# Kernel optimization log

Hardware: AMD Instinct MI355X
Metric: run time of the kernel (lower is better)

Reference implementation:

```python
import jax, jax.numpy as jnp
import numpy as np

N_HEAD = 16
SCALE = True


def setup_inputs() -> dict:
    key = jax.random.key(0)
    k1, k2, k3 = jax.random.split(key, 3)
    B, S, D = 4, 2048, 1024
    x = jax.random.normal(k1, (B, S, D), dtype=jnp.float32)
    w_attn = jax.random.normal(k2, (D, 3 * D), dtype=jnp.float32) * 0.02
    b_attn = jnp.zeros((3 * D,), dtype=jnp.float32)
    w_proj = jax.random.normal(k3, (D, D), dtype=jnp.float32) * 0.02
    b_proj = jnp.zeros((D,), dtype=jnp.float32)
    return {"x": x, "w_attn": w_attn, "b_attn": b_attn, "w_proj": w_proj, "b_proj": b_proj}


def reference(x, w_attn, b_attn, w_proj, b_proj):
    B, S, D = x.shape
    H = N_HEAD
    hd = D // H
    qkv = x @ w_attn + b_attn  # [B,S,3D] (Conv1D)
    q, k, v = jnp.split(qkv, 3, axis=-1)
    # split heads -> [B,H,S,hd]
    q = q.reshape(B, S, H, hd).transpose(0, 2, 1, 3)
    k = k.reshape(B, S, H, hd).transpose(0, 2, 1, 3)
    v = v.reshape(B, S, H, hd).transpose(0, 2, 1, 3)
    w = jnp.einsum('bhqd,bhkd->bhqk', q, k)  # [B,H,S,S]
    if SCALE:
        w = w / jnp.sqrt(jnp.asarray(hd, dtype=w.dtype))
    # causal mask exactly as in source: w*b + -10000*(1-b)
    bmask = jnp.tril(jnp.ones((S, S), dtype=w.dtype))[None, None]
    w = w * bmask + (-10000.0) * (1.0 - bmask)
    w = jax.nn.softmax(w, axis=-1)
    a = jnp.einsum('bhqk,bhkd->bhqd', w, v)  # [B,H,S,hd]
    a = a.transpose(0, 2, 1, 3).reshape(B, S, D)  # merge heads
    out = a @ w_proj + b_proj
    return out
```

## Files before the change

kernel.cpp:

```cpp
#include <hip/hip_runtime.h>

typedef __attribute__((ext_vector_type(8))) _Float16 f16x8;
typedef __attribute__((ext_vector_type(4))) float f32x4;

#define S_LEN 2048
#define DMODEL 1024
#define NHEAD 16
#define HD 64
#define QKV_LD 3072
#define BTOT 4
#define LOG2E 1.4426950408889634f

#define GLL16(g, l)                                              \
  __builtin_amdgcn_global_load_lds(                              \
      (const __attribute__((address_space(1))) void*)(g),        \
      (__attribute__((address_space(3))) void*)(l), 16, 0, 0)

#define MFMA16(a, b, c) __builtin_amdgcn_mfma_f32_16x16x32_f16(a, b, c, 0, 0, 0)

__global__ __launch_bounds__(256) void cvt_f32_f16_k(const float* __restrict__ in,
                                                     _Float16* __restrict__ out, int n) {
  int i = (blockIdx.x * 256 + threadIdx.x) * 4;
  int stride = gridDim.x * 256 * 4;
  for (; i < n; i += stride) {
    float4 v = *(const float4*)(in + i);
    _Float16 h[4];
    h[0] = (_Float16)v.x; h[1] = (_Float16)v.y; h[2] = (_Float16)v.z; h[3] = (_Float16)v.w;
    *(uint2*)(out + i) = *(const uint2*)h;
  }
}

__global__ __launch_bounds__(256) void transpose_cvt_k(const float* __restrict__ W,
                                                       _Float16* __restrict__ Wt,
                                                       int K, int N) {
  __shared__ float t[32][33];
  int n0 = blockIdx.x * 32, k0 = blockIdx.y * 32;
  int tx = threadIdx.x, ty = threadIdx.y;
#pragma unroll
  for (int i = 0; i < 32; i += 8)
    t[ty + i][tx] = W[(size_t)(k0 + ty + i) * N + n0 + tx];
  __syncthreads();
#pragma unroll
  for (int i = 0; i < 32; i += 8)
    Wt[(size_t)(n0 + ty + i) * K + k0 + tx] = (_Float16)t[tx][ty + i];
}

template <int OUT_F32>
__global__ __launch_bounds__(256) void gemm_bt_k(const _Float16* __restrict__ A,
                                                 const _Float16* __restrict__ Bt,
                                                 const float* __restrict__ bias,
                                                 void* __restrict__ C,
                                                 int M, int N, int K) {
  __shared__ _Float16 As[128 * 64];
  __shared__ _Float16 Bs[128 * 64];
  const int tid = threadIdx.x;
  const int wid = tid >> 6, lane = tid & 63;
  const int quad = lane >> 4, l16 = lane & 15;
  const int wr = wid >> 1, wc = wid & 1;

  const int lin = blockIdx.y * gridDim.x + blockIdx.x;
  const int width = 8 * gridDim.x;
  const int group = lin / width;
  const int pm = group * 8 + (lin % width) % 8;
  const int pn = (lin % width) / 8;
  const int tm = pm * 128, tn = pn * 128;

  const int row0 = tid >> 3;
  const int xc = 8 * ((tid & 7) ^ (row0 & 7));
  const _Float16* Ag = A + (size_t)(tm + row0) * K + xc;
  const _Float16* Bg = Bt + (size_t)(tn + row0) * K + xc;
  _Float16* AsW = &As[wid * 512];
  _Float16* BsW = &Bs[wid * 512];

  f32x4 acc[4][4] = {};

  for (int k0 = 0; k0 < K; k0 += 64) {
    __syncthreads();
#pragma unroll
    for (int p = 0; p < 4; p++) {
      GLL16(Ag + k0 + (size_t)(32 * p) * K, AsW + 2048 * p);
      GLL16(Bg + k0 + (size_t)(32 * p) * K, BsW + 2048 * p);
    }
    __syncthreads();

#pragma unroll
    for (int ks = 0; ks < 2; ks++) {
      f16x8 af[4], bf[4];
#pragma unroll
      for (int mt = 0; mt < 4; mt++)
        af[mt] = *(const f16x8*)&As[(wr * 64 + mt * 16 + l16) * 64 +
                                    (((ks * 4 + quad) ^ (l16 & 7)) << 3)];
#pragma unroll
      for (int nt = 0; nt < 4; nt++)
        bf[nt] = *(const f16x8*)&Bs[(wc * 64 + nt * 16 + l16) * 64 +
                                    (((ks * 4 + quad) ^ (l16 & 7)) << 3)];
#pragma unroll
      for (int mt = 0; mt < 4; mt++)
#pragma unroll
        for (int nt = 0; nt < 4; nt++)
          acc[mt][nt] = MFMA16(af[mt], bf[nt], acc[mt][nt]);
    }
  }

#pragma unroll
  for (int nt = 0; nt < 4; nt++) {
    int col = tn + wc * 64 + nt * 16 + l16;
    float bv = bias[col];
#pragma unroll
    for (int mt = 0; mt < 4; mt++) {
      int row = tm + wr * 64 + mt * 16 + quad * 4;
#pragma unroll
      for (int r = 0; r < 4; r++) {
        float v = acc[mt][nt][r] + bv;
        if (OUT_F32)
          ((float*)C)[(size_t)(row + r) * N + col] = v;
        else
          ((_Float16*)C)[(size_t)(row + r) * N + col] = (_Float16)v;
      }
    }
  }
}

__global__ __launch_bounds__(256, 3) void attn_k(const _Float16* __restrict__ qkv,
                                                 _Float16* __restrict__ out) {
  __shared__ _Float16 Ks[2][4096];
  __shared__ _Float16 VTs[2][4096];
  __shared__ _Float16 Ps[4][2304];

  const int tid = threadIdx.x, wid = tid >> 6, lane = tid & 63;
  const int quad = lane >> 4, l16 = lane & 15;
  const int bh = blockIdx.x, b = bh >> 4, h = bh & 15;
  const int p = blockIdx.y;
  const _Float16* base = qkv + (size_t)b * S_LEN * QKV_LD + h * HD;

  const int krow = tid >> 3;
  const _Float16* Kg = base + DMODEL + (size_t)krow * QKV_LD +
                       8 * ((tid & 7) ^ (krow & 7));
  const int kp = tid & 31, dbase = (tid >> 5) * 8;
  const _Float16* Vg = base + 2 * DMODEL + (size_t)(2 * kp) * QKV_LD + dbase;

  auto stage_V = [&](int bufi, uint4 v0, uint4 v1) {
    union { uint4 u; _Float16 h[8]; } a, c;
    a.u = v0; c.u = v1;
    uint* VT32 = (uint*)VTs[bufi];
#pragma unroll
    for (int i = 0; i < 8; i++) {
      int d = dbase + i;
      union { _Float16 h[2]; uint u; } w;
      w.h[0] = a.h[i]; w.h[1] = c.h[i];
      VT32[d * 32 + (((kp >> 2) ^ (d & 7)) << 2) + (kp & 3)] = w.u;
    }
  };

  auto run_pass = [&](int qt) {
    f16x8 bq[2][2];
    {
      const _Float16 qs = (_Float16)(0.125f * LOG2E);
#pragma unroll
      for (int nt = 0; nt < 2; nt++)
#pragma unroll
        for (int ks = 0; ks < 2; ks++) {
          union { uint4 u; f16x8 h; } v;
          v.u = *(const uint4*)(base + (size_t)(qt + wid * 32 + nt * 16 + l16) * QKV_LD +
                                ks * 32 + quad * 8);
          bq[nt][ks] = v.h * qs;
        }
    }

    float m_i[2] = {-1e30f, -1e30f}, l_i[2] = {0.f, 0.f};
    f32x4 o[4][2] = {};

    const int qmin_w = qt + wid * 32;
    const int qmax_w = qmin_w + 31;
    const int nj = qt / 64 + 2;

    GLL16(Kg, &Ks[0][wid * 512]);
    GLL16(Kg + (size_t)32 * QKV_LD, &Ks[0][2048 + wid * 512]);
    stage_V(0, *(const uint4*)(Vg), *(const uint4*)(Vg + QKV_LD));
    __syncthreads();

    for (int j = 0; j < nj; j++) {
      const int cur = j & 1, nxt = cur ^ 1;
      const int k0g = j * 64;
      const bool pf = (j + 1 < nj);
      uint4 pv0, pv1;
      if (pf) {
        const int kn = k0g + 64;
        GLL16(Kg + (size_t)kn * QKV_LD, &Ks[nxt][wid * 512]);
        GLL16(Kg + (size_t)(kn + 32) * QKV_LD, &Ks[nxt][2048 + wid * 512]);
        pv0 = *(const uint4*)(Vg + (size_t)kn * QKV_LD);
        pv1 = *(const uint4*)(Vg + (size_t)(kn + 1) * QKV_LD);
      }

      if (k0g <= qmax_w) {
        f32x4 sc[4][2] = {};
#pragma unroll
        for (int ks = 0; ks < 2; ks++) {
#pragma unroll
          for (int mt = 0; mt < 4; mt++) {
            f16x8 ak = *(const f16x8*)&Ks[cur][(mt * 16 + l16) * 64 +
                                               (((ks * 4 + quad) ^ (l16 & 7)) << 3)];
            sc[mt][0] = MFMA16(ak, bq[0][ks], sc[mt][0]);
            sc[mt][1] = MFMA16(ak, bq[1][ks], sc[mt][1]);
          }
        }

        const bool need_mask = (k0g + 63 > qmin_w);
        float alpha[2];
#pragma unroll
        for (int nt = 0; nt < 2; nt++) {
          const int qg = qmin_w + nt * 16 + l16;
          float s[16];
#pragma unroll
          for (int mt = 0; mt < 4; mt++)
#pragma unroll
            for (int r = 0; r < 4; r++) {
              float v = sc[mt][nt][r];
              if (need_mask) {
                int kg = k0g + mt * 16 + quad * 4 + r;
                v = (kg <= qg) ? v : -3.0e38f;
              }
              s[mt * 4 + r] = v;
            }
          float mx = s[0];
#pragma unroll
          for (int i = 1; i < 16; i++) mx = fmaxf(mx, s[i]);
          mx = fmaxf(mx, __shfl_xor(mx, 16, 64));
          mx = fmaxf(mx, __shfl_xor(mx, 32, 64));
          float mnew = fmaxf(m_i[nt], mx);
          alpha[nt] = __builtin_amdgcn_exp2f(m_i[nt] - mnew);
          m_i[nt] = mnew;
          float rs = 0.f;
          _Float16 ph[16];
#pragma unroll
          for (int i = 0; i < 16; i++) {
            float pv = __builtin_amdgcn_exp2f(s[i] - mnew);
            rs += pv;
            ph[i] = (_Float16)pv;
          }
          rs += __shfl_xor(rs, 16, 64);
          rs += __shfl_xor(rs, 32, 64);
          l_i[nt] = l_i[nt] * alpha[nt] + rs;
#pragma unroll
          for (int mt = 0; mt < 4; mt++)
            *(uint2*)&Ps[wid][(nt * 16 + l16) * 72 + mt * 16 + quad * 4] =
                *(uint2*)&ph[mt * 4];
        }
#pragma unroll
        for (int md = 0; md < 4; md++) {
          o[md][0] *= alpha[0];
          o[md][1] *= alpha[1];
        }
#pragma unroll
        for (int ks = 0; ks < 2; ks++) {
          f16x8 bp0 = *(const f16x8*)&Ps[wid][l16 * 72 + ks * 32 + quad * 8];
          f16x8 bp1 = *(const f16x8*)&Ps[wid][(16 + l16) * 72 + ks * 32 + quad * 8];
#pragma unroll
          for (int md = 0; md < 4; md++) {
            f16x8 av = *(const f16x8*)&VTs[cur][(md * 16 + l16) * 64 +
                                                (((ks * 4 + quad) ^ (l16 & 7)) << 3)];
            o[md][0] = MFMA16(av, bp0, o[md][0]);
            o[md][1] = MFMA16(av, bp1, o[md][1]);
          }
        }
      }

      if (pf) stage_V(nxt, pv0, pv1);
      __syncthreads();
    }

#pragma unroll
    for (int nt = 0; nt < 2; nt++) {
      float inv = 1.0f / l_i[nt];
#pragma unroll
      for (int md = 0; md < 4; md++) {
        _Float16 hh[4];
#pragma unroll
        for (int r = 0; r < 4; r++) hh[r] = (_Float16)(o[md][nt][r] * inv);
        *(uint2*)&Ps[wid][(nt * 16 + l16) * 72 + md * 16 + quad * 4] = *(uint2*)hh;
      }
    }
    {
      int r = lane >> 1, ch = (lane & 1) * 32;
      const int qg = qt + wid * 32 + r;
      _Float16* orow = out + (size_t)(b * S_LEN + qg) * DMODEL + h * HD + ch;
#pragma unroll
      for (int i = 0; i < 4; i++)
        *(uint4*)(orow + i * 8) = *(const uint4*)&Ps[wid][r * 72 + ch + i * 8];
    }
  };

  run_pass(p * 128);
  run_pass((15 - p) * 128);
}

extern "C" void kernel_launch(void* const* d_in, const int* in_sizes, int n_in,
                              void* d_out, int out_size, void* d_ws, size_t ws_size,
                              hipStream_t stream) {
  const float* x = (const float*)d_in[0];
  const float* w_attn = (const float*)d_in[1];
  const float* b_attn = (const float*)d_in[2];
  const float* w_proj = (const float*)d_in[3];
  const float* b_proj = (const float*)d_in[4];
  float* outp = (float*)d_out;

  char* ws = (char*)d_ws;
  _Float16* x16 = (_Float16*)ws;
  _Float16* wTa = (_Float16*)(ws + 16777216);
  _Float16* wTp = (_Float16*)(ws + 16777216 + 6291456);
  _Float16* qkv = (_Float16*)(ws + 25165824);
  _Float16* abuf = (_Float16*)(ws + 75497472);

  const int nx = BTOT * S_LEN * DMODEL;

  cvt_f32_f16_k<<<8192, 256, 0, stream>>>(x, x16, nx);
  transpose_cvt_k<<<dim3(QKV_LD / 32, DMODEL / 32), dim3(32, 8), 0, stream>>>(
      w_attn, wTa, DMODEL, QKV_LD);
  transpose_cvt_k<<<dim3(DMODEL / 32, DMODEL / 32), dim3(32, 8), 0, stream>>>(
      w_proj, wTp, DMODEL, DMODEL);

  gemm_bt_k<0><<<dim3(QKV_LD / 128, BTOT * S_LEN / 128), 256, 0, stream>>>(
      x16, wTa, b_attn, qkv, BTOT * S_LEN, QKV_LD, DMODEL);

  attn_k<<<dim3(BTOT * NHEAD, 8), 256, 0, stream>>>(qkv, abuf);

  gemm_bt_k<1><<<dim3(DMODEL / 128, BTOT * S_LEN / 128), 256, 0, stream>>>(
      abuf, wTp, b_proj, outp, BTOT * S_LEN, DMODEL, DMODEL);
}
```

Before: 282.8 us.

## Split attention across eight waves of 16 queries with lazy softmax rescaling

The attention kernel moves from 4 waves handling 32 query rows each to 8 waves handling 16 rows each, with 512 threads per block. K loading is spread over all waves, and V transposed staging is done by the first half of the threads. Rescaling of the online softmax is skipped unless the running max grows by more than a threshold across the whole wave. Conversions now use packed round-toward-zero f16. This adds parallelism and cuts per-wave registers, at the cost of fewer MFMAs per K/V LDS load and more waves sharing each barrier.

```diff
diff --git a/kernel.cpp b/kernel.cpp
--- a/kernel.cpp
+++ b/kernel.cpp
@@ -1,6 +1,7 @@
 #include <hip/hip_runtime.h>
 
 typedef __attribute__((ext_vector_type(8))) _Float16 f16x8;
+typedef __attribute__((ext_vector_type(2))) __fp16 h16x2;
 typedef __attribute__((ext_vector_type(4))) float f32x4;
 
 #define S_LEN 2048
@@ -121,11 +122,11 @@
   }
 }
 
-__global__ __launch_bounds__(256, 3) void attn_k(const _Float16* __restrict__ qkv,
+__global__ __launch_bounds__(512, 4) void attn_k(const _Float16* __restrict__ qkv,
                                                  _Float16* __restrict__ out) {
   __shared__ _Float16 Ks[2][4096];
   __shared__ _Float16 VTs[2][4096];
-  __shared__ _Float16 Ps[4][2304];
+  __shared__ _Float16 Ps[8][1152];
 
   const int tid = threadIdx.x, wid = tid >> 6, lane = tid & 63;
   const int quad = lane >> 4, l16 = lane & 15;
@@ -136,7 +137,8 @@
   const int krow = tid >> 3;
   const _Float16* Kg = base + DMODEL + (size_t)krow * QKV_LD +
                        8 * ((tid & 7) ^ (krow & 7));
-  const int kp = tid & 31, dbase = (tid >> 5) * 8;
+  const bool vstager = (tid < 256);
+  const int kp = tid & 31, dbase = ((tid >> 5) & 7) * 8;
   const _Float16* Vg = base + 2 * DMODEL + (size_t)(2 * kp) * QKV_LD + dbase;
 
   auto stage_V = [&](int bufi, uint4 v0, uint4 v1) {
@@ -153,30 +155,27 @@
   };
 
   auto run_pass = [&](int qt) {
-    f16x8 bq[2][2];
+    f16x8 bq[2];
     {
       const _Float16 qs = (_Float16)(0.125f * LOG2E);
 #pragma unroll
-      for (int nt = 0; nt < 2; nt++)
-#pragma unroll
-        for (int ks = 0; ks < 2; ks++) {
-          union { uint4 u; f16x8 h; } v;
-          v.u = *(const uint4*)(base + (size_t)(qt + wid * 32 + nt * 16 + l16) * QKV_LD +
-                                ks * 32 + quad * 8);
-          bq[nt][ks] = v.h * qs;
-        }
-    }
-
-    float m_i[2] = {-1e30f, -1e30f}, l_i[2] = {0.f, 0.f};
-    f32x4 o[4][2] = {};
-
-    const int qmin_w = qt + wid * 32;
-    const int qmax_w = qmin_w + 31;
+      for (int ks = 0; ks < 2; ks++) {
+        union { uint4 u; f16x8 h; } v;
+        v.u = *(const uint4*)(base + (size_t)(qt + wid * 16 + l16) * QKV_LD +
+                              ks * 32 + quad * 8);
+        bq[ks] = v.h * qs;
+      }
+    }
+
+    float m_i = -1e30f, l_i = 0.f;
+    f32x4 o[4] = {};
+
+    const int qmin_w = qt + wid * 16;
+    const int qmax_w = qmin_w + 15;
     const int nj = qt / 64 + 2;
 
     GLL16(Kg, &Ks[0][wid * 512]);
-    GLL16(Kg + (size_t)32 * QKV_LD, &Ks[0][2048 + wid * 512]);
-    stage_V(0, *(const uint4*)(Vg), *(const uint4*)(Vg + QKV_LD));
+    if (vstager) stage_V(0, *(const uint4*)(Vg), *(const uint4*)(Vg + QKV_LD));
     __syncthreads();
 
     for (int j = 0; j < nj; j++) {
@@ -187,106 +186,106 @@
       if (pf) {
         const int kn = k0g + 64;
         GLL16(Kg + (size_t)kn * QKV_LD, &Ks[nxt][wid * 512]);
-        GLL16(Kg + (size_t)(kn + 32) * QKV_LD, &Ks[nxt][2048 + wid * 512]);
-        pv0 = *(const uint4*)(Vg + (size_t)kn * QKV_LD);
-        pv1 = *(const uint4*)(Vg + (size_t)(kn + 1) * QKV_LD);
+        if (vstager) {
+          pv0 = *(const uint4*)(Vg + (size_t)kn * QKV_LD);
+          pv1 = *(const uint4*)(Vg + (size_t)(kn + 1) * QKV_LD);
+        }
       }
 
       if (k0g <= qmax_w) {
-        f32x4 sc[4][2] = {};
-#pragma unroll
-        for (int ks = 0; ks < 2; ks++) {
+        f32x4 sc[4] = {};
+#pragma unroll
+        for (int ks = 0; ks < 2; ks++)
 #pragma unroll
           for (int mt = 0; mt < 4; mt++) {
             f16x8 ak = *(const f16x8*)&Ks[cur][(mt * 16 + l16) * 64 +
                                                (((ks * 4 + quad) ^ (l16 & 7)) << 3)];
-            sc[mt][0] = MFMA16(ak, bq[0][ks], sc[mt][0]);
-            sc[mt][1] = MFMA16(ak, bq[1][ks], sc[mt][1]);
+            sc[mt] = MFMA16(ak, bq[ks], sc[mt]);
           }
+
+        const bool need_mask = (k0g + 63 > qmin_w);
+        const int qg = qmin_w + l16;
+        float s[16];
+#pragma unroll
+        for (int mt = 0; mt < 4; mt++)
+#pragma unroll
+          for (int r = 0; r < 4; r++) {
+            float v = sc[mt][r];
+            if (need_mask) {
+              int kg = k0g + mt * 16 + quad * 4 + r;
+              v = (kg <= qg) ? v : -3.0e38f;
+            }
+            s[mt * 4 + r] = v;
+          }
+        float t0 = fmaxf(fmaxf(s[0], s[1]), s[2]);
+        float t1 = fmaxf(fmaxf(s[3], s[4]), s[5]);
+        float t2 = fmaxf(fmaxf(s[6], s[7]), s[8]);
+        float t3 = fmaxf(fmaxf(s[9], s[10]), s[11]);
+        float t4 = fmaxf(fmaxf(s[12], s[13]), s[14]);
+        float mx = fmaxf(fmaxf(t0, t1), t2);
+        float my = fmaxf(fmaxf(t3, t4), s[15]);
+        mx = fmaxf(mx, my);
+        mx = fmaxf(mx, __shfl_xor(mx, 16, 64));
+        mx = fmaxf(mx, __shfl_xor(mx, 32, 64));
+
+        if (!__all(mx <= m_i + 8.0f)) {
+          float mnew = fmaxf(m_i, mx);
+          float alpha = __builtin_amdgcn_exp2f(m_i - mnew);
+          m_i = mnew;
+          l_i *= alpha;
+#pragma unroll
+          for (int md = 0; md < 4; md++) o[md] *= alpha;
         }
 
-        const bool need_mask = (k0g + 63 > qmin_w);
-        float alpha[2];
-#pragma unroll
-        for (int nt = 0; nt < 2; nt++) {
-          const int qg = qmin_w + nt * 16 + l16;
-          float s[16];
-#pragma unroll
-          for (int mt = 0; mt < 4; mt++)
-#pragma unroll
-            for (int r = 0; r < 4; r++) {
-              float v = sc[mt][nt][r];
-              if (need_mask) {
-                int kg = k0g + mt * 16 + quad * 4 + r;
-                v = (kg <= qg) ? v : -3.0e38f;
-              }
-              s[mt * 4 + r] = v;
-            }
-          float mx = s[0];
-#pragma unroll
-          for (int i = 1; i < 16; i++) mx = fmaxf(mx, s[i]);
-          mx = fmaxf(mx, __shfl_xor(mx, 16, 64));
-          mx = fmaxf(mx, __shfl_xor(mx, 32, 64));
-          float mnew = fmaxf(m_i[nt], mx);
-          alpha[nt] = __builtin_amdgcn_exp2f(m_i[nt] - mnew);
-          m_i[nt] = mnew;
-          float rs = 0.f;
-          _Float16 ph[16];
-#pragma unroll
-          for (int i = 0; i < 16; i++) {
-            float pv = __builtin_amdgcn_exp2f(s[i] - mnew);
-            rs += pv;
-            ph[i] = (_Float16)pv;
-          }
-          rs += __shfl_xor(rs, 16, 64);
-          rs += __shfl_xor(rs, 32, 64);
-          l_i[nt] = l_i[nt] * alpha[nt] + rs;
-#pragma unroll
-          for (int mt = 0; mt < 4; mt++)
-            *(uint2*)&Ps[wid][(nt * 16 + l16) * 72 + mt * 16 + quad * 4] =
-                *(uint2*)&ph[mt * 4];
+        float pe[16];
+#pragma unroll
+        for (int i = 0; i < 16; i++) pe[i] = __builtin_amdgcn_exp2f(s[i] - m_i);
+        float rs = ((pe[0] + pe[1]) + (pe[2] + pe[3])) +
+                   ((pe[4] + pe[5]) + (pe[6] + pe[7])) +
+                   (((pe[8] + pe[9]) + (pe[10] + pe[11])) +
+                    ((pe[12] + pe[13]) + (pe[14] + pe[15])));
+        rs += __shfl_xor(rs, 16, 64);
+        rs += __shfl_xor(rs, 32, 64);
+        l_i += rs;
+
+#pragma unroll
+        for (int mt = 0; mt < 4; mt++) {
+          union { h16x2 h[2]; uint2 u; } w;
+          w.h[0] = __builtin_amdgcn_cvt_pkrtz(pe[mt * 4 + 0], pe[mt * 4 + 1]);
+          w.h[1] = __builtin_amdgcn_cvt_pkrtz(pe[mt * 4 + 2], pe[mt * 4 + 3]);
+          *(uint2*)&Ps[wid][l16 * 72 + mt * 16 + quad * 4] = w.u;
         }
 #pragma unroll
-        for (int md = 0; md < 4; md++) {
-          o[md][0] *= alpha[0];
-          o[md][1] *= alpha[1];
-        }
-#pragma unroll
         for (int ks = 0; ks < 2; ks++) {
-          f16x8 bp0 = *(const f16x8*)&Ps[wid][l16 * 72 + ks * 32 + quad * 8];
-          f16x8 bp1 = *(const f16x8*)&Ps[wid][(16 + l16) * 72 + ks * 32 + quad * 8];
+          f16x8 bp = *(const f16x8*)&Ps[wid][l16 * 72 + ks * 32 + quad * 8];
 #pragma unroll
           for (int md = 0; md < 4; md++) {
             f16x8 av = *(const f16x8*)&VTs[cur][(md * 16 + l16) * 64 +
                                                 (((ks * 4 + quad) ^ (l16 & 7)) << 3)];
-            o[md][0] = MFMA16(av, bp0, o[md][0]);
-            o[md][1] = MFMA16(av, bp1, o[md][1]);
+            o[md] = MFMA16(av, bp, o[md]);
           }
         }
       }
 
-      if (pf) stage_V(nxt, pv0, pv1);
+      if (pf && vstager) stage_V(nxt, pv0, pv1);
       __syncthreads();
     }
 
-#pragma unroll
-    for (int nt = 0; nt < 2; nt++) {
-      float inv = 1.0f / l_i[nt];
+    {
+      float inv = 1.0f / l_i;
 #pragma unroll
       for (int md = 0; md < 4; md++) {
-        _Float16 hh[4];
-#pragma unroll
-        for (int r = 0; r < 4; r++) hh[r] = (_Float16)(o[md][nt][r] * inv);
-        *(uint2*)&Ps[wid][(nt * 16 + l16) * 72 + md * 16 + quad * 4] = *(uint2*)hh;
-      }
-    }
-    {
-      int r = lane >> 1, ch = (lane & 1) * 32;
-      const int qg = qt + wid * 32 + r;
-      _Float16* orow = out + (size_t)(b * S_LEN + qg) * DMODEL + h * HD + ch;
-#pragma unroll
-      for (int i = 0; i < 4; i++)
-        *(uint4*)(orow + i * 8) = *(const uint4*)&Ps[wid][r * 72 + ch + i * 8];
+        union { h16x2 h[2]; uint2 u; } w;
+        w.h[0] = __builtin_amdgcn_cvt_pkrtz(o[md][0] * inv, o[md][1] * inv);
+        w.h[1] = __builtin_amdgcn_cvt_pkrtz(o[md][2] * inv, o[md][3] * inv);
+        *(uint2*)&Ps[wid][l16 * 72 + md * 16 + quad * 4] = w.u;
+      }
+      int r = lane >> 2, cc = (lane & 3) * 16;
+      const int qg = qt + wid * 16 + r;
+      _Float16* orow = out + (size_t)(b * S_LEN + qg) * DMODEL + h * HD + cc;
+#pragma unroll
+      for (int i = 0; i < 2; i++)
+        *(uint4*)(orow + i * 8) = *(const uint4*)&Ps[wid][r * 72 + cc + i * 8];
     }
   };
 
@@ -322,7 +321,7 @@
   gemm_bt_k<0><<<dim3(QKV_LD / 128, BTOT * S_LEN / 128), 256, 0, stream>>>(
       x16, wTa, b_attn, qkv, BTOT * S_LEN, QKV_LD, DMODEL);
 
-  attn_k<<<dim3(BTOT * NHEAD, 8), 256, 0, stream>>>(qkv, abuf);
+  attn_k<<<dim3(BTOT * NHEAD, 8), 512, 0, stream>>>(qkv, abuf);
 
   gemm_bt_k<1><<<dim3(DMODEL / 128, BTOT * S_LEN / 128), 256, 0, stream>>>(
       abuf, wTp, b_proj, outp, BTOT * S_LEN, DMODEL, DMODEL);
```

After: 275.1 us. 2.7% less time.

## Split paired attention passes into one tile per block with lazy softmax rescale

Applied to the files above, without the earlier changes.

The attention kernel now launches 16 blocks per head, each handling one 128-row query tile, with the largest tiles scheduled first. Previously each block ran two balanced passes. This gives more blocks to fill the CUs but relies on the scheduler for causal load balance. Softmax rescaling now happens only when a wave's row max grows by more than 8 (in log2 units), skipping exp and multiplies on most iterations at the cost of larger unnormalized fp16 values. It also uses packed round-toward-zero conversions, a tree-shaped max/sum, and precomputed V transpose offsets.

```diff
diff --git a/kernel.cpp b/kernel.cpp
--- a/kernel.cpp
+++ b/kernel.cpp
@@ -1,6 +1,7 @@
 #include <hip/hip_runtime.h>
 
 typedef __attribute__((ext_vector_type(8))) _Float16 f16x8;
+typedef __attribute__((ext_vector_type(2))) __fp16 h16x2;
 typedef __attribute__((ext_vector_type(4))) float f32x4;
 
 #define S_LEN 2048
@@ -130,7 +131,8 @@
   const int tid = threadIdx.x, wid = tid >> 6, lane = tid & 63;
   const int quad = lane >> 4, l16 = lane & 15;
   const int bh = blockIdx.x, b = bh >> 4, h = bh & 15;
-  const int p = blockIdx.y;
+  const int tile = 15 - blockIdx.y;
+  const int qt = tile * 128;
   const _Float16* base = qkv + (size_t)b * S_LEN * QKV_LD + h * HD;
 
   const int krow = tid >> 3;
@@ -139,159 +141,180 @@
   const int kp = tid & 31, dbase = (tid >> 5) * 8;
   const _Float16* Vg = base + 2 * DMODEL + (size_t)(2 * kp) * QKV_LD + dbase;
 
+  int voff[8];
+#pragma unroll
+  for (int i = 0; i < 8; i++) {
+    int d = dbase + i;
+    voff[i] = d * 32 + (((kp >> 2) ^ (d & 7)) << 2) + (kp & 3);
+  }
+
   auto stage_V = [&](int bufi, uint4 v0, uint4 v1) {
     union { uint4 u; _Float16 h[8]; } a, c;
     a.u = v0; c.u = v1;
     uint* VT32 = (uint*)VTs[bufi];
 #pragma unroll
     for (int i = 0; i < 8; i++) {
-      int d = dbase + i;
       union { _Float16 h[2]; uint u; } w;
       w.h[0] = a.h[i]; w.h[1] = c.h[i];
-      VT32[d * 32 + (((kp >> 2) ^ (d & 7)) << 2) + (kp & 3)] = w.u;
+      VT32[voff[i]] = w.u;
     }
   };
 
-  auto run_pass = [&](int qt) {
-    f16x8 bq[2][2];
-    {
-      const _Float16 qs = (_Float16)(0.125f * LOG2E);
-#pragma unroll
-      for (int nt = 0; nt < 2; nt++)
-#pragma unroll
-        for (int ks = 0; ks < 2; ks++) {
-          union { uint4 u; f16x8 h; } v;
-          v.u = *(const uint4*)(base + (size_t)(qt + wid * 32 + nt * 16 + l16) * QKV_LD +
-                                ks * 32 + quad * 8);
-          bq[nt][ks] = v.h * qs;
+  f16x8 bq[2][2];
+  {
+    const _Float16 qs = (_Float16)(0.125f * LOG2E);
+#pragma unroll
+    for (int nt = 0; nt < 2; nt++)
+#pragma unroll
+      for (int ks = 0; ks < 2; ks++) {
+        union { uint4 u; f16x8 h; } v;
+        v.u = *(const uint4*)(base + (size_t)(qt + wid * 32 + nt * 16 + l16) * QKV_LD +
+                              ks * 32 + quad * 8);
+        bq[nt][ks] = v.h * qs;
+      }
+  }
+
+  float m_i[2] = {-1e30f, -1e30f}, l_i[2] = {0.f, 0.f};
+  f32x4 o[4][2] = {};
+
+  const int qmin_w = qt + wid * 32;
+  const int qmax_w = qmin_w + 31;
+  const int nj = qt / 64 + 2;
+
+  GLL16(Kg, &Ks[0][wid * 512]);
+  GLL16(Kg + (size_t)32 * QKV_LD, &Ks[0][2048 + wid * 512]);
+  stage_V(0, *(const uint4*)(Vg), *(const uint4*)(Vg + QKV_LD));
+  __syncthreads();
+
+  for (int j = 0; j < nj; j++) {
+    const int cur = j & 1, nxt = cur ^ 1;
+    const int k0g = j * 64;
+    const bool pf = (j + 1 < nj);
+    uint4 pv0, pv1;
+    if (pf) {
+      const int kn = k0g + 64;
+      GLL16(Kg + (size_t)kn * QKV_LD, &Ks[nxt][wid * 512]);
+      GLL16(Kg + (size_t)(kn + 32) * QKV_LD, &Ks[nxt][2048 + wid * 512]);
+      pv0 = *(const uint4*)(Vg + (size_t)kn * QKV_LD);
+      pv1 = *(const uint4*)(Vg + (size_t)(kn + 1) * QKV_LD);
+    }
+
+    if (k0g <= qmax_w) {
+      f32x4 sc[4][2] = {};
+#pragma unroll
+      for (int ks = 0; ks < 2; ks++) {
+#pragma unroll
+        for (int mt = 0; mt < 4; mt++) {
+          f16x8 ak = *(const f16x8*)&Ks[cur][(mt * 16 + l16) * 64 +
+                                             (((ks * 4 + quad) ^ (l16 & 7)) << 3)];
+          sc[mt][0] = MFMA16(ak, bq[0][ks], sc[mt][0]);
+          sc[mt][1] = MFMA16(ak, bq[1][ks], sc[mt][1]);
         }
-    }
-
-    float m_i[2] = {-1e30f, -1e30f}, l_i[2] = {0.f, 0.f};
-    f32x4 o[4][2] = {};
-
-    const int qmin_w = qt + wid * 32;
-    const int qmax_w = qmin_w + 31;
-    const int nj = qt / 64 + 2;
-
-    GLL16(Kg, &Ks[0][wid * 512]);
-    GLL16(Kg + (size_t)32 * QKV_LD, &Ks[0][2048 + wid * 512]);
-    stage_V(0, *(const uint4*)(Vg), *(const uint4*)(Vg + QKV_LD));
+      }
+
+      const bool need_mask = (k0g + 63 > qmin_w);
+      float s[2][16];
+      float mx[2];
+#pragma unroll
+      for (int nt = 0; nt < 2; nt++) {
+        const int qg = qmin_w + nt * 16 + l16;
+#pragma unroll
+        for (int mt = 0; mt < 4; mt++)
+#pragma unroll
+          for (int r = 0; r < 4; r++) {
+            float v = sc[mt][nt][r];
+            if (need_mask) {
+              int kg = k0g + mt * 16 + quad * 4 + r;
+              v = (kg <= qg) ? v : -3.0e38f;
+            }
+            s[nt][mt * 4 + r] = v;
+          }
+        float t0 = fmaxf(fmaxf(s[nt][0], s[nt][1]), s[nt][2]);
+        float t1 = fmaxf(fmaxf(s[nt][3], s[nt][4]), s[nt][5]);
+        float t2 = fmaxf(fmaxf(s[nt][6], s[nt][7]), s[nt][8]);
+        float t3 = fmaxf(fmaxf(s[nt][9], s[nt][10]), s[nt][11]);
+        float t4 = fmaxf(fmaxf(s[nt][12], s[nt][13]), s[nt][14]);
+        float m0 = fmaxf(fmaxf(t0, t1), t2);
+        float m1 = fmaxf(fmaxf(t3, t4), s[nt][15]);
+        float m = fmaxf(m0, m1);
+        m = fmaxf(m, __shfl_xor(m, 16, 64));
+        m = fmaxf(m, __shfl_xor(m, 32, 64));
+        mx[nt] = m;
+      }
+
+      bool grow = (mx[0] > m_i[0] + 8.0f) || (mx[1] > m_i[1] + 8.0f);
+      if (__any(grow)) {
+#pragma unroll
+        for (int nt = 0; nt < 2; nt++) {
+          float mnew = fmaxf(m_i[nt], mx[nt]);
+          float alpha = __builtin_amdgcn_exp2f(m_i[nt] - mnew);
+          m_i[nt] = mnew;
+          l_i[nt] *= alpha;
+#pragma unroll
+          for (int md = 0; md < 4; md++) o[md][nt] *= alpha;
+        }
+      }
+
+#pragma unroll
+      for (int nt = 0; nt < 2; nt++) {
+        float pe[16];
+#pragma unroll
+        for (int i = 0; i < 16; i++)
+          pe[i] = __builtin_amdgcn_exp2f(s[nt][i] - m_i[nt]);
+        float rs = ((pe[0] + pe[1]) + (pe[2] + pe[3])) +
+                   ((pe[4] + pe[5]) + (pe[6] + pe[7])) +
+                   (((pe[8] + pe[9]) + (pe[10] + pe[11])) +
+                    ((pe[12] + pe[13]) + (pe[14] + pe[15])));
+        rs += __shfl_xor(rs, 16, 64);
+        rs += __shfl_xor(rs, 32, 64);
+        l_i[nt] += rs;
+
+#pragma unroll
+        for (int mt = 0; mt < 4; mt++) {
+          union { h16x2 h[2]; uint2 u; } w;
+          w.h[0] = __builtin_amdgcn_cvt_pkrtz(pe[mt * 4 + 0], pe[mt * 4 + 1]);
+          w.h[1] = __builtin_amdgcn_cvt_pkrtz(pe[mt * 4 + 2], pe[mt * 4 + 3]);
+          *(uint2*)&Ps[wid][(nt * 16 + l16) * 72 + mt * 16 + quad * 4] = w.u;
+        }
+      }
+
+#pragma unroll
+      for (int ks = 0; ks < 2; ks++) {
+        f16x8 bp0 = *(const f16x8*)&Ps[wid][l16 * 72 + ks * 32 + quad * 8];
+        f16x8 bp1 = *(const f16x8*)&Ps[wid][(16 + l16) * 72 + ks * 32 + quad * 8];
+#pragma unroll
+        for (int md = 0; md < 4; md++) {
+          f16x8 av = *(const f16x8*)&VTs[cur][(md * 16 + l16) * 64 +
+                                              (((ks * 4 + quad) ^ (l16 & 7)) << 3)];
+          o[md][0] = MFMA16(av, bp0, o[md][0]);
+          o[md][1] = MFMA16(av, bp1, o[md][1]);
+        }
+      }
+    }
+
+    if (pf) stage_V(nxt, pv0, pv1);
     __syncthreads();
-
-    for (int j = 0; j < nj; j++) {
-      const int cur = j & 1, nxt = cur ^ 1;
-      const int k0g = j * 64;
-      const bool pf = (j + 1 < nj);
-      uint4 pv0, pv1;
-      if (pf) {
-        const int kn = k0g + 64;
-        GLL16(Kg + (size_t)kn * QKV_LD, &Ks[nxt][wid * 512]);
-        GLL16(Kg + (size_t)(kn + 32) * QKV_LD, &Ks[nxt][2048 + wid * 512]);
-        pv0 = *(const uint4*)(Vg + (size_t)kn * QKV_LD);
-        pv1 = *(const uint4*)(Vg + (size_t)(kn + 1) * QKV_LD);
-      }
-
-      if (k0g <= qmax_w) {
-        f32x4 sc[4][2] = {};
-#pragma unroll
-        for (int ks = 0; ks < 2; ks++) {
-#pragma unroll
-          for (int mt = 0; mt < 4; mt++) {
-            f16x8 ak = *(const f16x8*)&Ks[cur][(mt * 16 + l16) * 64 +
-                                               (((ks * 4 + quad) ^ (l16 & 7)) << 3)];
-            sc[mt][0] = MFMA16(ak, bq[0][ks], sc[mt][0]);
-            sc[mt][1] = MFMA16(ak, bq[1][ks], sc[mt][1]);
-          }
-        }
-
-        const bool need_mask = (k0g + 63 > qmin_w);
-        float alpha[2];
-#pragma unroll
-        for (int nt = 0; nt < 2; nt++) {
-          const int qg = qmin_w + nt * 16 + l16;
-          float s[16];
-#pragma unroll
-          for (int mt = 0; mt < 4; mt++)
-#pragma unroll
-            for (int r = 0; r < 4; r++) {
-              float v = sc[mt][nt][r];
-              if (need_mask) {
-                int kg = k0g + mt * 16 + quad * 4 + r;
-                v = (kg <= qg) ? v : -3.0e38f;
-              }
-              s[mt * 4 + r] = v;
-            }
-          float mx = s[0];
-#pragma unroll
-          for (int i = 1; i < 16; i++) mx = fmaxf(mx, s[i]);
-          mx = fmaxf(mx, __shfl_xor(mx, 16, 64));
-          mx = fmaxf(mx, __shfl_xor(mx, 32, 64));
-          float mnew = fmaxf(m_i[nt], mx);
-          alpha[nt] = __builtin_amdgcn_exp2f(m_i[nt] - mnew);
-          m_i[nt] = mnew;
-          float rs = 0.f;
-          _Float16 ph[16];
-#pragma unroll
-          for (int i = 0; i < 16; i++) {
-            float pv = __builtin_amdgcn_exp2f(s[i] - mnew);
-            rs += pv;
-            ph[i] = (_Float16)pv;
-          }
-          rs += __shfl_xor(rs, 16, 64);
-          rs += __shfl_xor(rs, 32, 64);
-          l_i[nt] = l_i[nt] * alpha[nt] + rs;
-#pragma unroll
-          for (int mt = 0; mt < 4; mt++)
-            *(uint2*)&Ps[wid][(nt * 16 + l16) * 72 + mt * 16 + quad * 4] =
-                *(uint2*)&ph[mt * 4];
-        }
-#pragma unroll
-        for (int md = 0; md < 4; md++) {
-          o[md][0] *= alpha[0];
-          o[md][1] *= alpha[1];
-        }
-#pragma unroll
-        for (int ks = 0; ks < 2; ks++) {
-          f16x8 bp0 = *(const f16x8*)&Ps[wid][l16 * 72 + ks * 32 + quad * 8];
-          f16x8 bp1 = *(const f16x8*)&Ps[wid][(16 + l16) * 72 + ks * 32 + quad * 8];
-#pragma unroll
-          for (int md = 0; md < 4; md++) {
-            f16x8 av = *(const f16x8*)&VTs[cur][(md * 16 + l16) * 64 +
-                                                (((ks * 4 + quad) ^ (l16 & 7)) << 3)];
-            o[md][0] = MFMA16(av, bp0, o[md][0]);
-            o[md][1] = MFMA16(av, bp1, o[md][1]);
-          }
-        }
-      }
-
-      if (pf) stage_V(nxt, pv0, pv1);
-      __syncthreads();
-    }
-
-#pragma unroll
-    for (int nt = 0; nt < 2; nt++) {
-      float inv = 1.0f / l_i[nt];
-#pragma unroll
-      for (int md = 0; md < 4; md++) {
-        _Float16 hh[4];
-#pragma unroll
-        for (int r = 0; r < 4; r++) hh[r] = (_Float16)(o[md][nt][r] * inv);
-        *(uint2*)&Ps[wid][(nt * 16 + l16) * 72 + md * 16 + quad * 4] = *(uint2*)hh;
-      }
-    }
-    {
-      int r = lane >> 1, ch = (lane & 1) * 32;
-      const int qg = qt + wid * 32 + r;
-      _Float16* orow = out + (size_t)(b * S_LEN + qg) * DMODEL + h * HD + ch;
-#pragma unroll
-      for (int i = 0; i < 4; i++)
-        *(uint4*)(orow + i * 8) = *(const uint4*)&Ps[wid][r * 72 + ch + i * 8];
-    }
-  };
-
-  run_pass(p * 128);
-  run_pass((15 - p) * 128);
+  }
+
+#pragma unroll
+  for (int nt = 0; nt < 2; nt++) {
+    float inv = 1.0f / l_i[nt];
+#pragma unroll
+    for (int md = 0; md < 4; md++) {
+      union { h16x2 h[2]; uint2 u; } w;
+      w.h[0] = __builtin_amdgcn_cvt_pkrtz(o[md][nt][0] * inv, o[md][nt][1] * inv);
+      w.h[1] = __builtin_amdgcn_cvt_pkrtz(o[md][nt][2] * inv, o[md][nt][3] * inv);
+      *(uint2*)&Ps[wid][(nt * 16 + l16) * 72 + md * 16 + quad * 4] = w.u;
+    }
+  }
+  {
+    int r = lane >> 1, ch = (lane & 1) * 32;
+    const int qg = qt + wid * 32 + r;
+    _Float16* orow = out + (size_t)(b * S_LEN + qg) * DMODEL + h * HD + ch;
+#pragma unroll
+    for (int i = 0; i < 4; i++)
+      *(uint4*)(orow + i * 8) = *(const uint4*)&Ps[wid][r * 72 + ch + i * 8];
+  }
 }
 
 extern "C" void kernel_launch(void* const* d_in, const int* in_sizes, int n_in,
@@ -322,7 +345,7 @@
   gemm_bt_k<0><<<dim3(QKV_LD / 128, BTOT * S_LEN / 128), 256, 0, stream>>>(
       x16, wTa, b_attn, qkv, BTOT * S_LEN, QKV_LD, DMODEL);
 
-  attn_k<<<dim3(BTOT * NHEAD, 8), 256, 0, stream>>>(qkv, abuf);
+  attn_k<<<dim3(BTOT * NHEAD, 16), 256, 0, stream>>>(qkv, abuf);
 
   gemm_bt_k<1><<<dim3(DMODEL / 128, BTOT * S_LEN / 128), 256, 0, stream>>>(
       abuf, wTp, b_proj, outp, BTOT * S_LEN, DMODEL, DMODEL);
```

New measurement: 269.6 us. 4.7% less time.
